# Kernel tuning notes

Measured on AMD Instinct MI355X. Metric: run time of the kernel, lower is better.

## Reference

```python
import jax, jax.numpy as jnp
import numpy as np

B, G, K, C, NT = 128, 64, 32, 256, 8192


def setup_inputs() -> dict:
    key = jax.random.key(0)
    ks = jax.random.split(key, 8)
    s = lambda fan_in: 1.0 / np.sqrt(fan_in)
    return {
        "patch_features": jax.random.normal(ks[0], (B, G, C), jnp.float32),
        "neighborhood": jax.random.normal(ks[1], (B, G, K, 3), jnp.float32),
        "codebook": jax.random.normal(ks[2], (NT, C), jnp.float32),
        "w1": jax.random.normal(ks[3], (512, C), jnp.float32) * s(C),
        "b1": jnp.zeros((512,), jnp.float32),
        "w2": jax.random.normal(ks[4], (256, 512), jnp.float32) * s(512),
        "b2": jnp.zeros((256,), jnp.float32),
        "w3": jax.random.normal(ks[5], (3 * K, 256), jnp.float32) * s(256),
        "b3": jnp.zeros((3 * K,), jnp.float32),
    }


def reference(patch_features, neighborhood, codebook, w1, b1, w2, b2, w3, b3):
    b, g, c = patch_features.shape
    k = neighborhood.shape[2]
    # squared euclidean distances to codebook (argmin equals argmin of cdist p=2)
    d2 = (
        jnp.sum(patch_features * patch_features, -1, keepdims=True)
        - 2.0 * jnp.einsum("bgc,nc->bgn", patch_features, codebook)
        + jnp.sum(codebook * codebook, -1)
    )  # [B,G,NT]
    token_ids = jnp.argmin(d2, axis=-1)          # [B,G]
    quantized = codebook[token_ids]              # [B,G,C] gather
    # 1x1 Conv1d stack == per-token MLP
    h = jax.nn.relu(jnp.einsum("bgc,oc->bgo", quantized, w1) + b1)
    h = jax.nn.relu(jnp.einsum("bgc,oc->bgo", h, w2) + b2)
    rec = jnp.einsum("bgc,oc->bgo", h, w3) + b3  # [B,G,3K]
    rec = rec.reshape(b * g, k, 3)
    gt = neighborhood.reshape(b * g, k, 3)
    # Chamfer distance L2 (squared) both directions
    diff = rec[:, :, None, :] - gt[:, None, :, :]  # [BG,K,K,3]
    dd = jnp.sum(diff * diff, -1)                  # [BG,K,K]
    loss = jnp.mean(jnp.min(dd, axis=2)) + jnp.mean(jnp.min(dd, axis=1))
    return loss
```

## Files before the change

### kernel.cpp

```cpp
#include <hip/hip_runtime.h>
#include <hip/hip_bf16.h>
#include <float.h>

#define NTOK 8192
#define NCB  8192
#define CDIM 256
#define KPTS 32
#define SQNT 24.0f
#define INV_CFOLD (SQNT * SQNT * 64.0f)

#define CG   8
#define TW   32

typedef __attribute__((ext_vector_type(8))) short short8;
typedef __attribute__((ext_vector_type(4))) float f32x4;
typedef __attribute__((ext_vector_type(4))) int i32x4;
typedef __attribute__((ext_vector_type(16))) int i32x16;
typedef unsigned int u32;
typedef unsigned long long u64;

__device__ __forceinline__ ushort bf16_rne(float x) {
  u32 u = __float_as_uint(x);
  return (ushort)((u + 0x7fffu + ((u >> 16) & 1u)) >> 16);
}

__device__ __forceinline__ int pack4i8(int a, int b, int c, int d) {
  return (a & 0xff) | ((b & 0xff) << 8) | ((c & 0xff) << 16) | ((d & 0xff) << 24);
}

__global__ __launch_bounds__(256) void prep_k(
    const float* __restrict__ pf, const float* __restrict__ cb,
    const float* __restrict__ w1, const float* __restrict__ w2,
    const float* __restrict__ w3,
    i32x4* __restrict__ pf1, i32x4* __restrict__ pf2,
    i32x4* __restrict__ cb1, i32x4* __restrict__ cb2,
    ushort* __restrict__ cb_bf, ushort* __restrict__ w1s,
    ushort* __restrict__ w2s, ushort* __restrict__ w3s,
    float* __restrict__ cnorm, float* __restrict__ out) {
  __shared__ float cred[4][16];
  if (blockIdx.x == 0 && threadIdx.x == 0) out[0] = 0.f;
  int gid = blockIdx.x * 4 + (threadIdx.x >> 6);
  int wv = threadIdx.x >> 6;
  int lane = threadIdx.x & 63, r16 = lane & 15, quad = lane >> 4;
  if (gid < 4096) {
    bool is_cb = gid >= 2048;
    int t = is_cb ? gid - 2048 : gid;
    int tile = t >> 2, kb = t & 3;
    const float* src = is_cb ? cb : pf;
    int row = tile * 16 + r16;
    const float* sp = src + (size_t)row * CDIM + kb * 64 + quad * 16;
    float4 v0 = ((const float4*)sp)[0];
    float4 v1 = ((const float4*)sp)[1];
    float4 v2 = ((const float4*)sp)[2];
    float4 v3 = ((const float4*)sp)[3];
    float x[16] = {v0.x, v0.y, v0.z, v0.w, v1.x, v1.y, v1.z, v1.w,
                   v2.x, v2.y, v2.z, v2.w, v3.x, v3.y, v3.z, v3.w};
    int q1[16], q2[16];
    float s = 0.f;
#pragma unroll
    for (int e = 0; e < 16; e++) {
      float as = x[e] * SQNT;
      float a1 = rintf(as);
      a1 = fminf(fmaxf(a1, -127.f), 127.f);
      float a2 = rintf((as - a1) * 128.f);
      a2 = fminf(fmaxf(a2, -127.f), 127.f);
      q1[e] = (int)a1;
      q2[e] = (int)a2;
      s += x[e] * x[e];
    }
    i32x4 p1 = {pack4i8(q1[0], q1[1], q1[2], q1[3]),
                pack4i8(q1[4], q1[5], q1[6], q1[7]),
                pack4i8(q1[8], q1[9], q1[10], q1[11]),
                pack4i8(q1[12], q1[13], q1[14], q1[15])};
    i32x4 p2 = {pack4i8(q2[0], q2[1], q2[2], q2[3]),
                pack4i8(q2[4], q2[5], q2[6], q2[7]),
                pack4i8(q2[8], q2[9], q2[10], q2[11]),
                pack4i8(q2[12], q2[13], q2[14], q2[15])};
    int rt32 = tile >> 1;
    int row_in = ((tile & 1) << 4) | r16;
    int kc32 = (kb << 1) | (quad >> 1);
    int k_half = quad & 1;
    size_t o = (size_t)(rt32 * 8 + kc32) * 64 + k_half * 32 + row_in;
    (is_cb ? cb1 : pf1)[o] = p1;
    (is_cb ? cb2 : pf2)[o] = p2;
    if (is_cb) {
      int kb32 = 2 * kb + (quad >> 1);
      int slot0 = ((2 * quad) & 3) * 16 + r16;
      int slot1 = ((2 * quad + 1) & 3) * 16 + r16;
      size_t bo = ((size_t)tile * 8 + kb32) * 512;
      short8 vh0 = {(short)bf16_rne(x[0]), (short)bf16_rne(x[1]),
                    (short)bf16_rne(x[2]), (short)bf16_rne(x[3]),
                    (short)bf16_rne(x[4]), (short)bf16_rne(x[5]),
                    (short)bf16_rne(x[6]), (short)bf16_rne(x[7])};
      short8 vh1 = {(short)bf16_rne(x[8]), (short)bf16_rne(x[9]),
                    (short)bf16_rne(x[10]), (short)bf16_rne(x[11]),
                    (short)bf16_rne(x[12]), (short)bf16_rne(x[13]),
                    (short)bf16_rne(x[14]), (short)bf16_rne(x[15])};
      *(short8*)(cb_bf + bo + (size_t)slot0 * 8) = vh0;
      *(short8*)(cb_bf + bo + (size_t)slot1 * 8) = vh1;
      s += __shfl_xor(s, 16, 64);
      s += __shfl_xor(s, 32, 64);
      if (quad == 0) cred[wv][r16] = s;
      __syncthreads();
      if (threadIdx.x < 16) {
        int ctile = blockIdx.x - 512;
        cnorm[ctile * 16 + threadIdx.x] =
            cred[0][threadIdx.x] + cred[1][threadIdx.x] +
            cred[2][threadIdx.x] + cred[3][threadIdx.x];
      }
    }
  } else if (gid < 4656) {
    int t = gid - 4096;
    const float* src;
    ushort* dst;
    int KB;
    if (t < 256)      { src = w1; dst = w1s; KB = 8; }
    else if (t < 512) { src = w2; dst = w2s; KB = 16; t -= 256; }
    else              { src = w3; dst = w3s; KB = 8;  t -= 512; }
    int tile = t / KB, kb = t - tile * KB, K = KB * 32;
    int row = tile * 16 + r16;
    const float* sp = src + (size_t)row * K + kb * 32 + quad * 8;
    float4 a = ((const float4*)sp)[0];
    float4 b = ((const float4*)sp)[1];
    short8 vh = {(short)bf16_rne(a.x), (short)bf16_rne(a.y),
                 (short)bf16_rne(a.z), (short)bf16_rne(a.w),
                 (short)bf16_rne(b.x), (short)bf16_rne(b.y),
                 (short)bf16_rne(b.z), (short)bf16_rne(b.w)};
    *(short8*)(dst + ((size_t)tile * KB + kb) * 512 + lane * 8) = vh;
  }
}

__device__ __forceinline__ void loadh(const char* bb1, const char* bb2,
                                      int offb, i32x4 (&q1)[4], i32x4 (&q2)[4]) {
#pragma unroll
  for (int k = 0; k < 4; ++k) {
    q1[k] = *(const i32x4*)(bb1 + (size_t)(offb + k) * 1024);
    q2[k] = *(const i32x4*)(bb2 + (size_t)(offb + k) * 1024);
  }
}

template <int KB>
__device__ __forceinline__ void mfmah(const i32x4* a1, const i32x4* a2,
                                      const i32x4 (&q1)[4], const i32x4 (&q2)[4],
                                      i32x16& am, i32x16& ac) {
#pragma unroll
  for (int k = 0; k < 4; ++k) {
    am = __builtin_amdgcn_mfma_i32_32x32x32_i8(a1[KB + k], q1[k], am, 0, 0, 0);
    ac = __builtin_amdgcn_mfma_i32_32x32x32_i8(a1[KB + k], q2[k], ac, 0, 0, 0);
    ac = __builtin_amdgcn_mfma_i32_32x32x32_i8(a2[KB + k], q1[k], ac, 0, 0, 0);
  }
}

__global__ __launch_bounds__(256, 2) void argmin_k(
    const char* __restrict__ A1g, const char* __restrict__ A2g,
    const char* __restrict__ B1g, const char* __restrict__ B2g,
    const float* __restrict__ cnorm, u64* __restrict__ pkeys) {
  __shared__ int cni_lds[1024];
  int tid = threadIdx.x;
  int cg = blockIdx.x, mt = blockIdx.y;
  int wv = tid >> 6, lane = tid & 63;
  int l31 = lane & 31, lh = lane >> 5;

  for (int k = tid; k < 1024; k += 256)
    cni_lds[k] = __float2int_rn(cnorm[cg * 1024 + k] * INV_CFOLD);

  i32x4 a1[8], a2[8];
  {
    int rtg = mt * 4 + wv;
    const char* a1p = A1g + (size_t)rtg * 8192 + (size_t)lane * 16;
    const char* a2p = A2g + (size_t)rtg * 8192 + (size_t)lane * 16;
#pragma unroll
    for (int kc = 0; kc < 8; ++kc) {
      a1[kc] = *(const i32x4*)(a1p + kc * 1024);
      a2[kc] = *(const i32x4*)(a2p + kc * 1024);
    }
#pragma unroll
    for (int kc = 0; kc < 8; ++kc) {
      asm volatile("" : "+v"(a1[kc]));
      asm volatile("" : "+v"(a2[kc]));
    }
  }
  __syncthreads();

  int bvi[16], bii[16];
#pragma unroll
  for (int r = 0; r < 16; ++r) { bvi[r] = 0x7fffffff; bii[r] = 0x7fffffff; }

  const char* bb1 = B1g + (size_t)(cg * TW) * 8192 + (size_t)lane * 16;
  const char* bb2 = B2g + (size_t)(cg * TW) * 8192 + (size_t)lane * 16;

  i32x4 q1A[4], q2A[4], q1B[4], q2B[4];
  i32x16 am, ac;

  loadh(bb1, bb2, 0, q1A, q2A);
  loadh(bb1, bb2, 4, q1B, q2B);

  for (int t = 0; t < TW - 1; ++t) {
#pragma unroll
    for (int r = 0; r < 16; ++r) { am[r] = 0; ac[r] = 0; }
    mfmah<0>(a1, a2, q1A, q2A, am, ac);
    loadh(bb1, bb2, (t + 1) * 8, q1A, q2A);
    mfmah<4>(a1, a2, q1B, q2B, am, ac);
    loadh(bb1, bb2, (t + 1) * 8 + 4, q1B, q2B);
    int cni = cni_lds[t * 32 + l31];
    int col = cg * 1024 + t * 32 + l31;
#pragma unroll
    for (int r = 0; r < 16; ++r) {
      int di = cni - (am[r] * 128 + ac[r]);
      if (di < bvi[r]) { bvi[r] = di; bii[r] = col; }
    }
  }
  {
    const int t = TW - 1;
#pragma unroll
    for (int r = 0; r < 16; ++r) { am[r] = 0; ac[r] = 0; }
    mfmah<0>(a1, a2, q1A, q2A, am, ac);
    mfmah<4>(a1, a2, q1B, q2B, am, ac);
    int cni = cni_lds[t * 32 + l31];
    int col = cg * 1024 + t * 32 + l31;
#pragma unroll
    for (int r = 0; r < 16; ++r) {
      int di = cni - (am[r] * 128 + ac[r]);
      if (di < bvi[r]) { bvi[r] = di; bii[r] = col; }
    }
  }

#pragma unroll
  for (int m = 1; m < 32; m <<= 1) {
#pragma unroll
    for (int r = 0; r < 16; ++r) {
      int ov = __shfl_xor(bvi[r], m, 64);
      int oi = __shfl_xor(bii[r], m, 64);
      if (ov < bvi[r] || (ov == bvi[r] && oi < bii[r])) {
        bvi[r] = ov;
        bii[r] = oi;
      }
    }
  }
  if (l31 == 0) {
    int rowb = mt * 128 + wv * 32 + 4 * lh;
    size_t sbase = (size_t)cg * NTOK;
#pragma unroll
    for (int r = 0; r < 16; ++r) {
      int row = rowb + (r & 3) + 8 * (r >> 2);
      u32 mk = (u32)(bvi[r] + (1 << 30));
      pkeys[sbase + row] = ((u64)mk << 32) | (u32)bii[r];
    }
  }
}

__global__ __launch_bounds__(512) void mlp_fused_k(
    const u64* __restrict__ pkeys, const ushort* __restrict__ cb_bf,
    const ushort* __restrict__ w1s, const float* __restrict__ b1,
    const ushort* __restrict__ w2s, const float* __restrict__ b2,
    const ushort* __restrict__ w3s, const float* __restrict__ b3,
    const float* __restrict__ neigh, float* __restrict__ out) {
  __shared__ ushort qs_h2[8 * 512];
  __shared__ ushort h1s[16 * 512];
  __shared__ float rec[16 * 96];
  __shared__ float gts[16 * 96];
  __shared__ int ids[16];
  __shared__ float wsum[8];

  int tid = threadIdx.x;
  int t0 = blockIdx.x * 16;
  int wv = tid >> 6, lane = tid & 63;
  int quad = lane >> 4, r16 = lane & 15;

  if (tid < 128) {
    int row_l = tid >> 3, sl = tid & 7;
    u64 best = pkeys[(size_t)sl * NTOK + t0 + row_l];
#pragma unroll
    for (int m = 1; m < 8; m <<= 1) {
      u64 o = __shfl_xor((unsigned long long)best, m, 64);
      if (o < best) best = o;
    }
    if (sl == 0) ids[row_l] = (int)(u32)best;
  }
  __syncthreads();

  {
    int kb = wv;
    int id = ids[r16];
    short8 v = *(const short8*)(cb_bf + ((size_t)(id >> 4) * 8 + kb) * 512 +
                                (size_t)((id & 15) + quad * 16) * 8);
    *(short8*)(qs_h2 + (size_t)kb * 512 + lane * 8) = v;
  }
  __syncthreads();

  short8 fa1[8];
#pragma unroll
  for (int kb = 0; kb < 8; kb++)
    fa1[kb] = *(const short8*)(qs_h2 + (size_t)kb * 512 + lane * 8);
  __syncthreads();

#pragma unroll
  for (int jj = 0; jj < 4; ++jj) {
    int jt = wv + jj * 8;
    f32x4 acc = (f32x4){0.f, 0.f, 0.f, 0.f};
#pragma unroll
    for (int kb = 0; kb < 8; kb++) {
      short8 fb = *(const short8*)(w1s + ((size_t)jt * 8 + kb) * 512 + lane * 8);
      acc = __builtin_amdgcn_mfma_f32_16x16x32_bf16(fa1[kb], fb, acc, 0, 0, 0);
    }
    int col = jt * 16 + r16;
    float bj = b1[col];
#pragma unroll
    for (int reg = 0; reg < 4; reg++) {
      int row_l = quad * 4 + reg;
      float v = fmaxf(acc[reg] + bj, 0.f);
      size_t o = (size_t)(col >> 5) * 512 +
                 (size_t)(((col >> 3) & 3) * 16 + row_l) * 8 + (col & 7);
      h1s[o] = bf16_rne(v);
    }
  }
  __syncthreads();

#pragma unroll
  for (int jj = 0; jj < 2; ++jj) {
    int jt = wv + jj * 8;
    f32x4 acc = (f32x4){0.f, 0.f, 0.f, 0.f};
#pragma unroll
    for (int kb = 0; kb < 16; kb++) {
      short8 fa = *(const short8*)(h1s + (size_t)kb * 512 + lane * 8);
      short8 fb = *(const short8*)(w2s + ((size_t)jt * 16 + kb) * 512 + lane * 8);
      acc = __builtin_amdgcn_mfma_f32_16x16x32_bf16(fa, fb, acc, 0, 0, 0);
    }
    int col = jt * 16 + r16;
    float bj = b2[col];
#pragma unroll
    for (int reg = 0; reg < 4; reg++) {
      int row_l = quad * 4 + reg;
      float v = fmaxf(acc[reg] + bj, 0.f);
      size_t o = (size_t)(col >> 5) * 512 +
                 (size_t)(((col >> 3) & 3) * 16 + row_l) * 8 + (col & 7);
      qs_h2[o] = bf16_rne(v);
    }
  }
  __syncthreads();

  if (tid < 384) {
    int t = tid / 24, c = (tid - t * 24) * 4;
    *(float4*)(gts + (size_t)t * 96 + c) =
        *(const float4*)(neigh + (size_t)(t0 + t) * 96 + c);
  }

  if (wv < 6) {
    int jt = wv;
    f32x4 acc = (f32x4){0.f, 0.f, 0.f, 0.f};
#pragma unroll
    for (int kb = 0; kb < 8; kb++) {
      short8 fa = *(const short8*)(qs_h2 + (size_t)kb * 512 + lane * 8);
      short8 fb = *(const short8*)(w3s + ((size_t)jt * 8 + kb) * 512 + lane * 8);
      acc = __builtin_amdgcn_mfma_f32_16x16x32_bf16(fa, fb, acc, 0, 0, 0);
    }
    int col = jt * 16 + r16;
    float bj = b3[col];
#pragma unroll
    for (int reg = 0; reg < 4; reg++) {
      int row_l = quad * 4 + reg;
      rec[(size_t)row_l * 96 + col] = acc[reg] + bj;
    }
  }
  __syncthreads();

  float local = 0.f;
  {
    int t = tid >> 5, i = tid & 31;
    float rx = rec[t * 96 + 3 * i], ry = rec[t * 96 + 3 * i + 1], rz = rec[t * 96 + 3 * i + 2];
    float gx = gts[t * 96 + 3 * i], gy = gts[t * 96 + 3 * i + 1], gz = gts[t * 96 + 3 * i + 2];
    float mA = FLT_MAX, mB = FLT_MAX;
#pragma unroll
    for (int j = 0; j < 32; j++) {
      float dx = rx - gts[t * 96 + 3 * j], dy = ry - gts[t * 96 + 3 * j + 1],
            dz = rz - gts[t * 96 + 3 * j + 2];
      float d = dx * dx + dy * dy + dz * dz;
      mA = fminf(mA, d);
      dx = rec[t * 96 + 3 * j] - gx; dy = rec[t * 96 + 3 * j + 1] - gy;
      dz = rec[t * 96 + 3 * j + 2] - gz;
      d = dx * dx + dy * dy + dz * dz;
      mB = fminf(mB, d);
    }
    local = mA + mB;
  }
#pragma unroll
  for (int off = 32; off; off >>= 1) local += __shfl_down(local, off, 64);
  if (lane == 0) wsum[wv] = local;
  __syncthreads();
  if (tid == 0) {
    float s = 0.f;
#pragma unroll
    for (int w = 0; w < 8; w++) s += wsum[w];
    atomicAdd(out, s * (1.0f / (float)(NTOK * KPTS)));
  }
}

extern "C" void kernel_launch(void* const* d_in, const int* in_sizes, int n_in,
                              void* d_out, int out_size, void* d_ws, size_t ws_size,
                              hipStream_t stream) {
  const float* pf    = (const float*)d_in[0];
  const float* neigh = (const float*)d_in[1];
  const float* cb    = (const float*)d_in[2];
  const float* w1    = (const float*)d_in[3];
  const float* b1    = (const float*)d_in[4];
  const float* w2    = (const float*)d_in[5];
  const float* b2    = (const float*)d_in[6];
  const float* w3    = (const float*)d_in[7];
  const float* b3    = (const float*)d_in[8];
  float* out = (float*)d_out;
  char* base = (char*)d_ws;

  u64*   pkeys = (u64*)base;
  float* cnorm = (float*)(base + 0x200000);
  char*  pf1   = base + 0x210000;
  char*  pf2   = base + 0x410000;
  char*  cb1   = base + 0x610000;
  char*  cb2   = base + 0x810000;
  ushort* cb_bf = (ushort*)(base + 0xA10000);
  ushort* w1s   = (ushort*)(base + 0xE10000);
  ushort* w2s   = (ushort*)(base + 0xE50000);
  ushort* w3s   = (ushort*)(base + 0xE90000);

  prep_k<<<1164, 256, 0, stream>>>(pf, cb, w1, w2, w3,
                                   (i32x4*)pf1, (i32x4*)pf2, (i32x4*)cb1,
                                   (i32x4*)cb2, cb_bf, w1s, w2s, w3s, cnorm, out);
  argmin_k<<<dim3(CG, 64), 256, 0, stream>>>(pf1, pf2, cb1, cb2, cnorm, pkeys);
  mlp_fused_k<<<512, 512, 0, stream>>>(pkeys, cb_bf, w1s, b1, w2s, b2,
                                       w3s, b3, neigh, out);
}
```

Baseline: 166.9 us.

## Restructure argmin tiling: share A rows via LDS, split codebook across waves

The argmin kernel now stages a 64-row token tile into LDS with direct global-to-LDS loads, and each wave processes two 32-row sub-tiles against its own slice of the codebook group. Before, each wave held its own 32 rows in registers and swept all columns. Per-wave argmins are merged through a shared cross array, and the grid doubles in the row dimension. This is meant to raise B-operand reuse (each codebook fragment feeds two row tiles) and deepen the prefetch pipeline. In exchange it adds LDS reads of A every step and an extra block-wide reduction and sync.

```diff
diff --git a/kernel.cpp b/kernel.cpp
--- a/kernel.cpp
+++ b/kernel.cpp
@@ -10,7 +10,6 @@
 #define INV_CFOLD (SQNT * SQNT * 64.0f)
 
 #define CG   8
-#define TW   32
 
 typedef __attribute__((ext_vector_type(8))) short short8;
 typedef __attribute__((ext_vector_type(4))) float f32x4;
@@ -18,6 +17,12 @@
 typedef __attribute__((ext_vector_type(16))) int i32x16;
 typedef unsigned int u32;
 typedef unsigned long long u64;
+
+__device__ __forceinline__ void gl_lds16(const void* g, void* l) {
+  __builtin_amdgcn_global_load_lds(
+      (const __attribute__((address_space(1))) u32*)(g),
+      (__attribute__((address_space(3))) u32*)(l), 16, 0, 0);
+}
 
 __device__ __forceinline__ ushort bf16_rne(float x) {
   u32 u = __float_as_uint(x);
@@ -130,122 +135,115 @@
   }
 }
 
-__device__ __forceinline__ void loadh(const char* bb1, const char* bb2,
-                                      int offb, i32x4 (&q1)[4], i32x4 (&q2)[4]) {
-#pragma unroll
-  for (int k = 0; k < 4; ++k) {
-    q1[k] = *(const i32x4*)(bb1 + (size_t)(offb + k) * 1024);
-    q2[k] = *(const i32x4*)(bb2 + (size_t)(offb + k) * 1024);
-  }
-}
-
-template <int KB>
-__device__ __forceinline__ void mfmah(const i32x4* a1, const i32x4* a2,
-                                      const i32x4 (&q1)[4], const i32x4 (&q2)[4],
-                                      i32x16& am, i32x16& ac) {
-#pragma unroll
-  for (int k = 0; k < 4; ++k) {
-    am = __builtin_amdgcn_mfma_i32_32x32x32_i8(a1[KB + k], q1[k], am, 0, 0, 0);
-    ac = __builtin_amdgcn_mfma_i32_32x32x32_i8(a1[KB + k], q2[k], ac, 0, 0, 0);
-    ac = __builtin_amdgcn_mfma_i32_32x32x32_i8(a2[KB + k], q1[k], ac, 0, 0, 0);
-  }
-}
-
 __global__ __launch_bounds__(256, 2) void argmin_k(
     const char* __restrict__ A1g, const char* __restrict__ A2g,
     const char* __restrict__ B1g, const char* __restrict__ B2g,
     const float* __restrict__ cnorm, u64* __restrict__ pkeys) {
+  __shared__ char a_lds[32768];
   __shared__ int cni_lds[1024];
+  __shared__ u64 cross[64][4];
   int tid = threadIdx.x;
   int cg = blockIdx.x, mt = blockIdx.y;
   int wv = tid >> 6, lane = tid & 63;
   int l31 = lane & 31, lh = lane >> 5;
 
+#pragma unroll
+  for (int u = 0; u < 8; ++u) {
+    int c = wv * 8 + u;
+    int lv = c >> 4, rs = (c >> 3) & 1, kc = c & 7;
+    const char* src = (lv ? A2g : A1g) +
+        (size_t)((mt * 2 + rs) * 8 + kc) * 1024 + (size_t)lane * 16;
+    gl_lds16(src, a_lds + c * 1024);
+  }
   for (int k = tid; k < 1024; k += 256)
     cni_lds[k] = __float2int_rn(cnorm[cg * 1024 + k] * INV_CFOLD);
-
-  i32x4 a1[8], a2[8];
-  {
-    int rtg = mt * 4 + wv;
-    const char* a1p = A1g + (size_t)rtg * 8192 + (size_t)lane * 16;
-    const char* a2p = A2g + (size_t)rtg * 8192 + (size_t)lane * 16;
-#pragma unroll
-    for (int kc = 0; kc < 8; ++kc) {
-      a1[kc] = *(const i32x4*)(a1p + kc * 1024);
-      a2[kc] = *(const i32x4*)(a2p + kc * 1024);
-    }
-#pragma unroll
-    for (int kc = 0; kc < 8; ++kc) {
-      asm volatile("" : "+v"(a1[kc]));
-      asm volatile("" : "+v"(a2[kc]));
-    }
-  }
-  __syncthreads();
-
-  int bvi[16], bii[16];
-#pragma unroll
-  for (int r = 0; r < 16; ++r) { bvi[r] = 0x7fffffff; bii[r] = 0x7fffffff; }
-
-  const char* bb1 = B1g + (size_t)(cg * TW) * 8192 + (size_t)lane * 16;
-  const char* bb2 = B2g + (size_t)(cg * TW) * 8192 + (size_t)lane * 16;
-
-  i32x4 q1A[4], q2A[4], q1B[4], q2B[4];
-  i32x16 am, ac;
-
-  loadh(bb1, bb2, 0, q1A, q2A);
-  loadh(bb1, bb2, 4, q1B, q2B);
-
-  for (int t = 0; t < TW - 1; ++t) {
-#pragma unroll
-    for (int r = 0; r < 16; ++r) { am[r] = 0; ac[r] = 0; }
-    mfmah<0>(a1, a2, q1A, q2A, am, ac);
-    loadh(bb1, bb2, (t + 1) * 8, q1A, q2A);
-    mfmah<4>(a1, a2, q1B, q2B, am, ac);
-    loadh(bb1, bb2, (t + 1) * 8 + 4, q1B, q2B);
-    int cni = cni_lds[t * 32 + l31];
-    int col = cg * 1024 + t * 32 + l31;
+  __syncthreads();
+
+  const char* ab  = a_lds + (size_t)lane * 16;
+  const char* bb1 = B1g + (size_t)(cg * 32 + wv * 8) * 8192 + (size_t)lane * 16;
+  const char* bb2 = B2g + (size_t)(cg * 32 + wv * 8) * 8192 + (size_t)lane * 16;
+
+  int bv0[16], bi0[16], bv1[16], bi1[16];
+#pragma unroll
+  for (int r = 0; r < 16; ++r) {
+    bv0[r] = 0x7fffffff; bi0[r] = 0x7fffffff;
+    bv1[r] = 0x7fffffff; bi1[r] = 0x7fffffff;
+  }
+
+  i32x4 r1[4], r2[4];
+#pragma unroll
+  for (int s = 0; s < 3; ++s) {
+    r1[s] = *(const i32x4*)(bb1 + (size_t)s * 1024);
+    r2[s] = *(const i32x4*)(bb2 + (size_t)s * 1024);
+  }
+
+  const i32x16 Z = {0, 0, 0, 0, 0, 0, 0, 0, 0, 0, 0, 0, 0, 0, 0, 0};
+  i32x16 am0, am1, ac0, ac1;
+
+#pragma unroll
+  for (int s = 0; s < 64; ++s) {
+    const int t = s >> 3, kc = s & 7, sl = s & 3, sp = (s + 3) & 3;
+    if (s + 3 < 64) {
+      r1[sp] = *(const i32x4*)(bb1 + (size_t)(s + 3) * 1024);
+      r2[sp] = *(const i32x4*)(bb2 + (size_t)(s + 3) * 1024);
+    }
+    i32x4 a10 = *(const i32x4*)(ab + (kc) * 1024);
+    i32x4 a11 = *(const i32x4*)(ab + (8 + kc) * 1024);
+    i32x4 a20 = *(const i32x4*)(ab + (16 + kc) * 1024);
+    i32x4 a21 = *(const i32x4*)(ab + (24 + kc) * 1024);
+    if (kc == 0) {
+      am0 = __builtin_amdgcn_mfma_i32_32x32x32_i8(a10, r1[sl], Z, 0, 0, 0);
+      am1 = __builtin_amdgcn_mfma_i32_32x32x32_i8(a11, r1[sl], Z, 0, 0, 0);
+      ac0 = __builtin_amdgcn_mfma_i32_32x32x32_i8(a10, r2[sl], Z, 0, 0, 0);
+      ac1 = __builtin_amdgcn_mfma_i32_32x32x32_i8(a11, r2[sl], Z, 0, 0, 0);
+      ac0 = __builtin_amdgcn_mfma_i32_32x32x32_i8(a20, r1[sl], ac0, 0, 0, 0);
+      ac1 = __builtin_amdgcn_mfma_i32_32x32x32_i8(a21, r1[sl], ac1, 0, 0, 0);
+    } else {
+      am0 = __builtin_amdgcn_mfma_i32_32x32x32_i8(a10, r1[sl], am0, 0, 0, 0);
+      am1 = __builtin_amdgcn_mfma_i32_32x32x32_i8(a11, r1[sl], am1, 0, 0, 0);
+      ac0 = __builtin_amdgcn_mfma_i32_32x32x32_i8(a10, r2[sl], ac0, 0, 0, 0);
+      ac1 = __builtin_amdgcn_mfma_i32_32x32x32_i8(a11, r2[sl], ac1, 0, 0, 0);
+      ac0 = __builtin_amdgcn_mfma_i32_32x32x32_i8(a20, r1[sl], ac0, 0, 0, 0);
+      ac1 = __builtin_amdgcn_mfma_i32_32x32x32_i8(a21, r1[sl], ac1, 0, 0, 0);
+    }
+    if (kc == 7) {
+      int ctl = wv * 8 + t;
+      int col = (cg * 32 + ctl) * 32 + l31;
+      int cni = cni_lds[ctl * 32 + l31];
+#pragma unroll
+      for (int r = 0; r < 16; ++r) {
+        int d0 = cni - (am0[r] * 128 + ac0[r]);
+        if (d0 < bv0[r]) { bv0[r] = d0; bi0[r] = col; }
+        int d1 = cni - (am1[r] * 128 + ac1[r]);
+        if (d1 < bv1[r]) { bv1[r] = d1; bi1[r] = col; }
+      }
+    }
+  }
+
+#pragma unroll
+  for (int m = 1; m < 32; m <<= 1) {
 #pragma unroll
     for (int r = 0; r < 16; ++r) {
-      int di = cni - (am[r] * 128 + ac[r]);
-      if (di < bvi[r]) { bvi[r] = di; bii[r] = col; }
-    }
-  }
-  {
-    const int t = TW - 1;
-#pragma unroll
-    for (int r = 0; r < 16; ++r) { am[r] = 0; ac[r] = 0; }
-    mfmah<0>(a1, a2, q1A, q2A, am, ac);
-    mfmah<4>(a1, a2, q1B, q2B, am, ac);
-    int cni = cni_lds[t * 32 + l31];
-    int col = cg * 1024 + t * 32 + l31;
+      int ov = __shfl_xor(bv0[r], m, 64), oi = __shfl_xor(bi0[r], m, 64);
+      if (ov < bv0[r] || (ov == bv0[r] && oi < bi0[r])) { bv0[r] = ov; bi0[r] = oi; }
+      ov = __shfl_xor(bv1[r], m, 64); oi = __shfl_xor(bi1[r], m, 64);
+      if (ov < bv1[r] || (ov == bv1[r] && oi < bi1[r])) { bv1[r] = ov; bi1[r] = oi; }
+    }
+  }
+  if (l31 == 0) {
 #pragma unroll
     for (int r = 0; r < 16; ++r) {
-      int di = cni - (am[r] * 128 + ac[r]);
-      if (di < bvi[r]) { bvi[r] = di; bii[r] = col; }
-    }
-  }
-
-#pragma unroll
-  for (int m = 1; m < 32; m <<= 1) {
-#pragma unroll
-    for (int r = 0; r < 16; ++r) {
-      int ov = __shfl_xor(bvi[r], m, 64);
-      int oi = __shfl_xor(bii[r], m, 64);
-      if (ov < bvi[r] || (ov == bvi[r] && oi < bii[r])) {
-        bvi[r] = ov;
-        bii[r] = oi;
-      }
-    }
-  }
-  if (l31 == 0) {
-    int rowb = mt * 128 + wv * 32 + 4 * lh;
-    size_t sbase = (size_t)cg * NTOK;
-#pragma unroll
-    for (int r = 0; r < 16; ++r) {
-      int row = rowb + (r & 3) + 8 * (r >> 2);
-      u32 mk = (u32)(bvi[r] + (1 << 30));
-      pkeys[sbase + row] = ((u64)mk << 32) | (u32)bii[r];
-    }
+      int crow = (r & 3) + 8 * (r >> 2) + 4 * lh;
+      cross[crow][wv]      = ((u64)(u32)(bv0[r] + (1 << 30)) << 32) | (u32)bi0[r];
+      cross[32 + crow][wv] = ((u64)(u32)(bv1[r] + (1 << 30)) << 32) | (u32)bi1[r];
+    }
+  }
+  __syncthreads();
+  if (tid < 64) {
+    u64 b = cross[tid][0];
+#pragma unroll
+    for (int w = 1; w < 4; ++w) { u64 o = cross[tid][w]; if (o < b) b = o; }
+    pkeys[(size_t)cg * NTOK + mt * 64 + tid] = b;
   }
 }
 
@@ -424,7 +422,7 @@
   prep_k<<<1164, 256, 0, stream>>>(pf, cb, w1, w2, w3,
                                    (i32x4*)pf1, (i32x4*)pf2, (i32x4*)cb1,
                                    (i32x4*)cb2, cb_bf, w1s, w2s, w3s, cnorm, out);
-  argmin_k<<<dim3(CG, 64), 256, 0, stream>>>(pf1, pf2, cb1, cb2, cnorm, pkeys);
+  argmin_k<<<dim3(CG, 128), 256, 0, stream>>>(pf1, pf2, cb1, cb2, cnorm, pkeys);
   mlp_fused_k<<<512, 512, 0, stream>>>(pkeys, cb_bf, w1s, b1, w2s, b2,
                                        w3s, b3, neigh, out);
 }
```

New measurement: 248.5 us. 1.49x slower.
